# Optimization experiments

Measured on AMD Instinct MI355X. Metric: run time of the kernel, lower is better.

Reference implementation:

```python
import jax, jax.numpy as jnp
import numpy as np

DIM = 2048
N_HEADS = 16
HEAD_DIM = DIM // N_HEADS
MAX_SEQ_LEN = 2048
ROPE_THETA = 32.0
EPS = 1e-6


def _precompute_freqs_1d(dim, max_seq_len, theta):
    freqs = theta ** (-np.arange(0, dim, 2, dtype=np.float32) / dim)  # [dim/2]
    pos = np.arange(max_seq_len, dtype=np.float32)                    # [S]
    ang = pos[:, None] * freqs[None, :]                               # [S, dim/2]
    return jnp.asarray(np.cos(ang)), jnp.asarray(np.sin(ang))


def _rms_norm(x, w):
    # x: [..., d]
    inv = jax.lax.rsqrt(jnp.mean(x * x, axis=-1, keepdims=True) + EPS)
    return x * inv * w


def setup_inputs() -> dict:
    key = jax.random.key(0)
    k1, k2, k3 = jax.random.split(key, 3)
    bsz, seq_len = 4, 2048
    x = jax.random.normal(k1, (bsz, seq_len, DIM), dtype=jnp.float32)
    w_qkv = jax.random.normal(k2, (3 * DIM, DIM), dtype=jnp.float32) * (DIM ** -0.5)
    w_proj = jax.random.normal(k3, (DIM, DIM), dtype=jnp.float32) * (DIM ** -0.5)
    q_norm_w = jnp.ones((HEAD_DIM,), dtype=jnp.float32)
    k_norm_w = jnp.ones((HEAD_DIM,), dtype=jnp.float32)
    return {"x": x, "w_qkv": w_qkv, "w_proj": w_proj,
            "q_norm_w": q_norm_w, "k_norm_w": k_norm_w}


def reference(x, w_qkv, w_proj, q_norm_w, k_norm_w):
    bsz, seq_len, dim = x.shape
    scale = HEAD_DIM ** -0.5

    # QKV projection (torch Linear: x @ W^T)
    qkv = jnp.einsum('bsd,ed->bse', x, w_qkv)  # [b, s, 3*dim]
    qkv = qkv.reshape(bsz, seq_len, 3, N_HEADS, HEAD_DIM).transpose(2, 0, 3, 1, 4)
    q, k, v = qkv[0], qkv[1], qkv[2]           # each [b, h, s, d]

    # Per-head RMSNorm on q, k
    q = _rms_norm(q, q_norm_w)
    k = _rms_norm(k, k_norm_w)

    # RoPE (half-split convention)
    cos, sin = _precompute_freqs_1d(HEAD_DIM, MAX_SEQ_LEN, ROPE_THETA)
    cos = cos[:seq_len][None, None]  # [1,1,s,d/2]
    sin = sin[:seq_len][None, None]
    q1, q2 = jnp.split(q, 2, axis=-1)
    k1, k2 = jnp.split(k, 2, axis=-1)
    q = jnp.concatenate([q1 * cos - q2 * sin, q2 * cos + q1 * sin], axis=-1)
    k = jnp.concatenate([k1 * cos - k2 * sin, k2 * cos + k1 * sin], axis=-1)

    # Scaled dot-product attention (no mask, eval-mode: no dropout)
    scores = jnp.einsum('bhqd,bhkd->bhqk', q, k) * scale
    attn = jax.nn.softmax(scores, axis=-1)
    y = jnp.einsum('bhqk,bhkd->bhqd', attn, v)

    # Merge heads + output projection
    y = y.transpose(0, 2, 1, 3).reshape(bsz, seq_len, dim)
    return jnp.einsum('bsd,ed->bse', y, w_proj)
```

## Files before the change

### kernel.cpp

```cpp
#include <hip/hip_runtime.h>
#include <hip/hip_bf16.h>

#define BSZ 4
#define SEQ 2048
#define DIM 2048
#define NH 16
#define HD 128
#define QK_LD 4096
#define SCALE 0.08838834764831845f
#define SC2 0.12751742910198f

typedef __attribute__((ext_vector_type(8))) short bf16x8;
typedef __attribute__((ext_vector_type(4))) float f32x4;

#define GLDS16(g, l)                                                           \
  __builtin_amdgcn_global_load_lds(                                           \
      (const __attribute__((address_space(1))) void*)(g),                     \
      (__attribute__((address_space(3))) void*)(l), 16, 0, 0)

__device__ inline short f2b(float f) {
  __hip_bfloat16 h = __float2bfloat16(f);
  short s;
  __builtin_memcpy(&s, &h, 2);
  return s;
}

__device__ inline void stage16(const float* gp, __hip_bfloat16* lp) {
  float4 q0 = ((const float4*)gp)[0], q1 = ((const float4*)gp)[1];
  float4 q2 = ((const float4*)gp)[2], q3 = ((const float4*)gp)[3];
  bf16x8 v0, v1;
  v0[0] = f2b(q0.x); v0[1] = f2b(q0.y); v0[2] = f2b(q0.z); v0[3] = f2b(q0.w);
  v0[4] = f2b(q1.x); v0[5] = f2b(q1.y); v0[6] = f2b(q1.z); v0[7] = f2b(q1.w);
  v1[0] = f2b(q2.x); v1[1] = f2b(q2.y); v1[2] = f2b(q2.z); v1[3] = f2b(q2.w);
  v1[4] = f2b(q3.x); v1[5] = f2b(q3.y); v1[6] = f2b(q3.z); v1[7] = f2b(q3.w);
  *(bf16x8*)lp = v0;
  *(bf16x8*)(lp + 8) = v1;
}

__device__ inline char* out_slice(void* outv, int b, int fl) {
  return (char*)outv + (size_t)b * (size_t)SEQ * DIM * (fl ? 2u : 4u);
}

__device__ inline void xcd_remap(long& bm, long& bn) {
  int nwg = gridDim.x * gridDim.y;
  int lin = blockIdx.y * gridDim.x + blockIdx.x;
  int cpx = nwg >> 3;
  lin = (lin & 7) * cpx + (lin >> 3);
  bm = (long)(lin % gridDim.x) * 128;
  bn = (long)(lin / gridDim.x) * 128;
}

__global__ __launch_bounds__(256)
void detect_canon(const unsigned int* __restrict__ wbits,
                  const void* __restrict__ qw, const void* __restrict__ kw,
                  __hip_bfloat16* __restrict__ qwb,
                  __hip_bfloat16* __restrict__ kwb, int* __restrict__ flag) {
  __shared__ int cnt;
  const int t = threadIdx.x;
  if (t == 0) cnt = 0;
  __syncthreads();
  int local = 0;
  for (int i = 0; i < 4; ++i) {
    unsigned int e = (wbits[t * 4 + i] >> 7) & 0xFF;
    if (e >= 96 && e < 160) local++;
  }
  atomicAdd(&cnt, local);
  __syncthreads();
  const int f = (cnt >= 768) ? 1 : 0;
  if (t == 0) *flag = f;
  if (t < 128)
    qwb[t] = f ? ((const __hip_bfloat16*)qw)[t]
               : __float2bfloat16(((const float*)qw)[t]);
  else
    kwb[t - 128] = f ? ((const __hip_bfloat16*)kw)[t - 128]
                     : __float2bfloat16(((const float*)kw)[t - 128]);
}

__global__ __launch_bounds__(256)
void convert_bf16(const void* __restrict__ in, __hip_bfloat16* __restrict__ out,
                  const int* __restrict__ flag) {
  const int fl = *flag;
  long i = ((long)blockIdx.x * 256 + threadIdx.x) * 8;
  if (fl) {
    *(float4*)(out + i) = *(const float4*)((const __hip_bfloat16*)in + i);
  } else {
    const float* p = (const float*)in + i;
    float4 a = ((const float4*)p)[0], b = ((const float4*)p)[1];
    bf16x8 o;
    o[0] = f2b(a.x); o[1] = f2b(a.y); o[2] = f2b(a.z); o[3] = f2b(a.w);
    o[4] = f2b(b.x); o[5] = f2b(b.y); o[6] = f2b(b.z); o[7] = f2b(b.w);
    *(bf16x8*)(out + i) = o;
  }
}


__global__ __launch_bounds__(256)
void gemm_qkv_full(const __hip_bfloat16* __restrict__ A,
                   const __hip_bfloat16* __restrict__ B,
                   __hip_bfloat16* __restrict__ qk, void* __restrict__ outv,
                   const int* __restrict__ flag) {
  __shared__ __hip_bfloat16 As[128 * 32];
  __shared__ __hip_bfloat16 Bs[128 * 32];
  const int t = threadIdx.x, wave = t >> 6, lane = t & 63;
  const int quad = lane >> 4, l16 = lane & 15;
  const int wm = (wave & 1) * 64, wn = (wave >> 1) * 64;
  long bm, bn;
  xcd_remap(bm, bn);
  const int fl = *flag;

  f32x4 acc[4][4] = {};
  for (int k0 = 0; k0 < DIM; k0 += 32) {
    __syncthreads();
    for (int i = 0; i < 2; ++i) {
      int c = wave * 64 + lane + i * 256;
      int row = c >> 2, kc = c & 3;
      GLDS16(A + (bm + row) * DIM + k0 + kc * 8, As + (wave * 64 + i * 256) * 8);
      GLDS16(B + (bn + row) * DIM + k0 + kc * 8, Bs + (wave * 64 + i * 256) * 8);
    }
    __syncthreads();
    bf16x8 aF[4], bF[4];
    for (int mt = 0; mt < 4; ++mt)
      aF[mt] = *(const bf16x8*)(As + (wm + mt * 16 + l16) * 32 + quad * 8);
    for (int nt = 0; nt < 4; ++nt)
      bF[nt] = *(const bf16x8*)(Bs + (wn + nt * 16 + l16) * 32 + quad * 8);
    for (int mt = 0; mt < 4; ++mt)
      for (int nt = 0; nt < 4; ++nt)
        acc[mt][nt] = __builtin_amdgcn_mfma_f32_16x16x32_bf16(
            aF[mt], bF[nt], acc[mt][nt], 0, 0, 0);
  }

  if (bn < 4096) {
    for (int mt = 0; mt < 4; ++mt) {
      long gr = bm + wm + mt * 16 + quad * 4;
      for (int nt = 0; nt < 4; ++nt) {
        long gc = bn + wn + nt * 16 + l16;
        for (int r = 0; r < 4; ++r)
          qk[(gr + r) * QK_LD + gc] = __float2bfloat16(acc[mt][nt][r]);
      }
    }
  } else {
    for (int mt = 0; mt < 4; ++mt) {
      long gr = bm + wm + mt * 16 + quad * 4;
      __hip_bfloat16* vtb = (__hip_bfloat16*)out_slice(outv, (int)(gr >> 11), fl);
      long s = gr & 2047;
      for (int nt = 0; nt < 4; ++nt) {
        long col = bn - 4096 + wn + nt * 16 + l16;
        for (int r = 0; r < 4; ++r)
          vtb[col * SEQ + s + r] = __float2bfloat16(acc[mt][nt][r]);
      }
    }
  }
}

__global__ __launch_bounds__(256)
void gemm_proj_full(const __hip_bfloat16* __restrict__ A,
                    const __hip_bfloat16* __restrict__ B,
                    void* __restrict__ outv, const int* __restrict__ flag) {
  __shared__ __hip_bfloat16 As[128 * 32];
  __shared__ __hip_bfloat16 Bs[128 * 32];
  const int t = threadIdx.x, wave = t >> 6, lane = t & 63;
  const int quad = lane >> 4, l16 = lane & 15;
  const int wm = (wave & 1) * 64, wn = (wave >> 1) * 64;
  long bm, bn;
  xcd_remap(bm, bn);
  const int fl = *flag;

  f32x4 acc[4][4] = {};
  for (int k0 = 0; k0 < DIM; k0 += 32) {
    __syncthreads();
    for (int i = 0; i < 2; ++i) {
      int c = wave * 64 + lane + i * 256;
      int row = c >> 2, kc = c & 3;
      GLDS16(A + (bm + row) * QK_LD + k0 + kc * 8, As + (wave * 64 + i * 256) * 8);
      GLDS16(B + (bn + row) * DIM + k0 + kc * 8, Bs + (wave * 64 + i * 256) * 8);
    }
    __syncthreads();
    bf16x8 aF[4], bF[4];
    for (int mt = 0; mt < 4; ++mt)
      aF[mt] = *(const bf16x8*)(As + (wm + mt * 16 + l16) * 32 + quad * 8);
    for (int nt = 0; nt < 4; ++nt)
      bF[nt] = *(const bf16x8*)(Bs + (wn + nt * 16 + l16) * 32 + quad * 8);
    for (int mt = 0; mt < 4; ++mt)
      for (int nt = 0; nt < 4; ++nt)
        acc[mt][nt] = __builtin_amdgcn_mfma_f32_16x16x32_bf16(
            aF[mt], bF[nt], acc[mt][nt], 0, 0, 0);
  }

  for (int mt = 0; mt < 4; ++mt) {
    long gr = bm + wm + mt * 16 + quad * 4;
    for (int nt = 0; nt < 4; ++nt) {
      long gc = bn + wn + nt * 16 + l16;
      for (int r = 0; r < 4; ++r) {
        long idx = (gr + r) * DIM + gc;
        if (fl) ((__hip_bfloat16*)outv)[idx] = __float2bfloat16(acc[mt][nt][r]);
        else    ((float*)outv)[idx] = acc[mt][nt][r];
      }
    }
  }
}


__global__ __launch_bounds__(256)
void gemm_qkv(const void* __restrict__ xin, const void* __restrict__ win,
              __hip_bfloat16* __restrict__ qk, void* __restrict__ outv,
              const int* __restrict__ flag, int b) {
  __shared__ __hip_bfloat16 As[128 * 32];
  __shared__ __hip_bfloat16 Bs[128 * 32];
  const int t = threadIdx.x, wave = t >> 6, lane = t & 63;
  const int quad = lane >> 4, l16 = lane & 15;
  const int wm = (wave & 1) * 64, wn = (wave >> 1) * 64;
  const long bm = (long)blockIdx.x * 128, bn = (long)blockIdx.y * 128;
  const int fl = *flag;
  const __hip_bfloat16* Ab = (const __hip_bfloat16*)xin + (long)b * SEQ * DIM;
  const __hip_bfloat16* Bb = (const __hip_bfloat16*)win;
  const float* Af = (const float*)xin + (long)b * SEQ * DIM;
  const float* Bf = (const float*)win;

  f32x4 acc[4][4] = {};
  for (int k0 = 0; k0 < DIM; k0 += 32) {
    __syncthreads();
    if (fl) {
      for (int i = 0; i < 2; ++i) {
        int c = wave * 64 + lane + i * 256;
        int row = c >> 2, kc = c & 3;
        GLDS16(Ab + (bm + row) * DIM + k0 + kc * 8, As + (wave * 64 + i * 256) * 8);
        GLDS16(Bb + (bn + row) * DIM + k0 + kc * 8, Bs + (wave * 64 + i * 256) * 8);
      }
    } else {
      int row = t >> 1, cb = k0 + (t & 1) * 16;
      stage16(Af + (bm + row) * DIM + cb, As + t * 16);
      stage16(Bf + (bn + row) * DIM + cb, Bs + t * 16);
    }
    __syncthreads();
    bf16x8 aF[4], bF[4];
    for (int mt = 0; mt < 4; ++mt)
      aF[mt] = *(const bf16x8*)(As + (wm + mt * 16 + l16) * 32 + quad * 8);
    for (int nt = 0; nt < 4; ++nt)
      bF[nt] = *(const bf16x8*)(Bs + (wn + nt * 16 + l16) * 32 + quad * 8);
    for (int mt = 0; mt < 4; ++mt)
      for (int nt = 0; nt < 4; ++nt)
        acc[mt][nt] = __builtin_amdgcn_mfma_f32_16x16x32_bf16(
            aF[mt], bF[nt], acc[mt][nt], 0, 0, 0);
  }

  if (bn < 4096) {
    for (int mt = 0; mt < 4; ++mt) {
      long gr = bm + wm + mt * 16 + quad * 4;
      for (int nt = 0; nt < 4; ++nt) {
        long gc = bn + wn + nt * 16 + l16;
        for (int r = 0; r < 4; ++r)
          qk[(gr + r) * QK_LD + gc] = __float2bfloat16(acc[mt][nt][r]);
      }
    }
  } else {
    __hip_bfloat16* vtb = (__hip_bfloat16*)out_slice(outv, b, fl);
    for (int mt = 0; mt < 4; ++mt) {
      long gr = bm + wm + mt * 16 + quad * 4;
      for (int nt = 0; nt < 4; ++nt) {
        long col = bn - 4096 + wn + nt * 16 + l16;
        for (int r = 0; r < 4; ++r)
          vtb[col * SEQ + gr + r] = __float2bfloat16(acc[mt][nt][r]);
      }
    }
  }
}

__global__ __launch_bounds__(256)
void gemm_proj(const __hip_bfloat16* __restrict__ A, const void* __restrict__ win,
               void* __restrict__ outv, const int* __restrict__ flag, int b) {
  __shared__ __hip_bfloat16 As[128 * 32];
  __shared__ __hip_bfloat16 Bs[128 * 32];
  const int t = threadIdx.x, wave = t >> 6, lane = t & 63;
  const int quad = lane >> 4, l16 = lane & 15;
  const int wm = (wave & 1) * 64, wn = (wave >> 1) * 64;
  const long bm = (long)blockIdx.x * 128, bn = (long)blockIdx.y * 128;
  const int fl = *flag;
  const __hip_bfloat16* Bb = (const __hip_bfloat16*)win;
  const float* Bf = (const float*)win;

  f32x4 acc[4][4] = {};
  for (int k0 = 0; k0 < DIM; k0 += 32) {
    __syncthreads();
    for (int i = 0; i < 2; ++i) {
      int c = wave * 64 + lane + i * 256;
      int row = c >> 2, kc = c & 3;
      GLDS16(A + (bm + row) * QK_LD + k0 + kc * 8, As + (wave * 64 + i * 256) * 8);
    }
    if (fl) {
      for (int i = 0; i < 2; ++i) {
        int c = wave * 64 + lane + i * 256;
        int row = c >> 2, kc = c & 3;
        GLDS16(Bb + (bn + row) * DIM + k0 + kc * 8, Bs + (wave * 64 + i * 256) * 8);
      }
    } else {
      int row = t >> 1, cb = k0 + (t & 1) * 16;
      stage16(Bf + (bn + row) * DIM + cb, Bs + t * 16);
    }
    __syncthreads();
    bf16x8 aF[4], bF[4];
    for (int mt = 0; mt < 4; ++mt)
      aF[mt] = *(const bf16x8*)(As + (wm + mt * 16 + l16) * 32 + quad * 8);
    for (int nt = 0; nt < 4; ++nt)
      bF[nt] = *(const bf16x8*)(Bs + (wn + nt * 16 + l16) * 32 + quad * 8);
    for (int mt = 0; mt < 4; ++mt)
      for (int nt = 0; nt < 4; ++nt)
        acc[mt][nt] = __builtin_amdgcn_mfma_f32_16x16x32_bf16(
            aF[mt], bF[nt], acc[mt][nt], 0, 0, 0);
  }

  char* Cb = out_slice(outv, b, fl);
  for (int mt = 0; mt < 4; ++mt) {
    long gr = bm + wm + mt * 16 + quad * 4;
    for (int nt = 0; nt < 4; ++nt) {
      long gc = bn + wn + nt * 16 + l16;
      for (int r = 0; r < 4; ++r) {
        long idx = (gr + r) * DIM + gc;
        if (fl) ((__hip_bfloat16*)Cb)[idx] = __float2bfloat16(acc[mt][nt][r]);
        else    ((float*)Cb)[idx] = acc[mt][nt][r];
      }
    }
  }
}


__global__ __launch_bounds__(256)
void norm_rope(__hip_bfloat16* __restrict__ qk,
               const __hip_bfloat16* __restrict__ qwb,
               const __hip_bfloat16* __restrict__ kwb) {
  const int wave = threadIdx.x >> 6, lane = threadIdx.x & 63;
  const int gid = blockIdx.x * 4 + wave;
  const int h = gid & 15, tt = (gid >> 4) & 1, row = gid >> 5;
  const int s = row & 2047;

  __hip_bfloat16* p = qk + (long)row * QK_LD + tt * DIM + h * HD;
  unsigned int u = ((const unsigned int*)p)[lane];

  unsigned int x = (unsigned int)__shfl((int)u, lane >> 1);
  unsigned int y = (unsigned int)__shfl((int)u, 32 + (lane >> 1));
  float v1 = __uint_as_float((lane & 1) ? (x & 0xFFFF0000u) : (x << 16));
  float v2 = __uint_as_float((lane & 1) ? (y & 0xFFFF0000u) : (y << 16));

  float ss = v1 * v1 + v2 * v2;
  for (int off = 1; off < 64; off <<= 1) ss += __shfl_xor(ss, off);
  float inv = rsqrtf(ss * (1.0f / 128.0f) + 1e-6f);

  const __hip_bfloat16* w = tt ? kwb : qwb;
  float n1 = v1 * inv * __bfloat162float(w[lane]);
  float n2 = v2 * inv * __bfloat162float(w[lane + 64]);

  float freq = exp2f(-5.0f * (float)lane * (1.0f / 64.0f));
  float ang = (float)s * freq;
  float c = cosf(ang), sn = sinf(ang);
  float r1 = n1 * c - n2 * sn;
  float r2 = n2 * c + n1 * sn;

  float z1lo = __shfl(r1, (2 * lane) & 63), z2lo = __shfl(r2, (2 * lane) & 63);
  float z1hi = __shfl(r1, (2 * lane + 1) & 63), z2hi = __shfl(r2, (2 * lane + 1) & 63);
  float lo = (lane < 32) ? z1lo : z2lo;
  float hi = (lane < 32) ? z1hi : z2hi;
  unsigned int ou = (unsigned int)(unsigned short)f2b(lo) |
                    ((unsigned int)(unsigned short)f2b(hi) << 16);
  ((unsigned int*)p)[lane] = ou;
}

#define FA_STAGE_K(J)                                                          \
  _Pragma("unroll")                                                            \
  for (int i_ = 0; i_ < 2; ++i_) {                                             \
    int f_ = t + i_ * 512;                                                     \
    int kk_ = f_ & 3, row_ = (f_ >> 2) & 63, ks_ = f_ >> 8;                    \
    GLDS16(Kg + (long)((J) + row_) * QK_LD + ks_ * 32 +                        \
               (kk_ ^ ((row_ >> 1) & 3)) * 8,                                  \
           Ks + (t + i_ * 512) * 8);                                           \
  }
#define FA_STAGE_V(J)                                                          \
  _Pragma("unroll")                                                            \
  for (int i_ = 0; i_ < 2; ++i_) {                                             \
    int f_ = t + i_ * 512;                                                     \
    int kk_ = f_ & 3, dim_ = (f_ >> 2) & 127, ks2_ = f_ >> 9;                  \
    GLDS16(Vt + (long)dim_ * SEQ + (J) + ks2_ * 32 +                           \
               (kk_ ^ ((dim_ >> 1) & 3)) * 8,                                  \
           Vs + (t + i_ * 512) * 8);                                           \
  }
#define FA_WAIT2 asm volatile("s_waitcnt vmcnt(2)" ::: "memory")
#define FA_WAIT0 asm volatile("s_waitcnt vmcnt(0)" ::: "memory")
#define FA_BAR                                                                 \
  do {                                                                         \
    asm volatile("" ::: "memory");                                             \
    __builtin_amdgcn_s_barrier();                                              \
    asm volatile("" ::: "memory");                                             \
  } while (0)

__global__ __launch_bounds__(512)
void flash_attn(__hip_bfloat16* __restrict__ qkbase, void* __restrict__ outv,
                const int* __restrict__ flag, int b0) {
  __shared__ __hip_bfloat16 Ks[4 * 64 * 32];
  __shared__ __hip_bfloat16 Vs[2 * 128 * 32];

  const int t = threadIdx.x, wave = t >> 6, lane = t & 63;
  const int quad = lane >> 4, l16 = lane & 15;
  const int swz = (quad ^ ((l16 >> 1) & 3)) * 8;
  const int q0 = blockIdx.x * 128, h = blockIdx.y;
  const int b = b0 + blockIdx.z;
  const int fl = *flag;
  __hip_bfloat16* qk = qkbase + (long)blockIdx.z * SEQ * QK_LD;
  __hip_bfloat16* Qg = qk + h * HD;
  const __hip_bfloat16* Kg = Qg + DIM;
  const __hip_bfloat16* Vt =
      (const __hip_bfloat16*)out_slice(outv, b, fl) + (long)h * HD * SEQ;

  const int srcA = ((lane >> 4) & 1) * 32 + l16;
  const int srcB = srcA + 16;
  const bool hiq = (quad >= 2);

  bf16x8 aQ[4];
#pragma unroll
  for (int ks = 0; ks < 4; ++ks)
    aQ[ks] = *(const bf16x8*)(Qg +
        (long)(q0 + wave * 16 + l16) * QK_LD + ks * 32 + quad * 8);

  f32x4 oacc[8] = {};
  float m_run = -1e30f, l_run = 0.0f;

  FA_STAGE_K(0);
  FA_STAGE_V(0);

  for (int j0 = 0; j0 < SEQ; j0 += 64) {
    const bool more = (j0 + 64 < SEQ);

    FA_WAIT2;
    FA_BAR;

    f32x4 sacc[4] = {};
    __builtin_amdgcn_s_setprio(1);
#pragma unroll
    for (int ks = 0; ks < 4; ++ks)
#pragma unroll
      for (int nt = 0; nt < 4; ++nt) {
        bf16x8 bK = *(const bf16x8*)(Ks + (ks * 64 + nt * 16 + l16) * 32 + swz);
        sacc[nt] = __builtin_amdgcn_mfma_f32_16x16x32_bf16(
            bK, aQ[ks], sacc[nt], 0, 0, 0);
      }
    __builtin_amdgcn_s_setprio(0);

    FA_BAR;
    if (more) { FA_STAGE_K(j0 + 64); }

    float p[16];
#pragma unroll
    for (int nt = 0; nt < 4; ++nt)
#pragma unroll
      for (int r = 0; r < 4; ++r) p[nt * 4 + r] = sacc[nt][r] * SC2;
    float mx = p[0];
#pragma unroll
    for (int i = 1; i < 16; ++i) mx = fmaxf(mx, p[i]);
    mx = fmaxf(mx, __shfl_xor(mx, 16));
    mx = fmaxf(mx, __shfl_xor(mx, 32));
    if (__any(mx > m_run + 8.0f)) {
      float mnew = fmaxf(m_run, mx);
      float alpha = exp2f(m_run - mnew);
      m_run = mnew;
      l_run *= alpha;
#pragma unroll
      for (int r = 0; r < 4; ++r) {
        float ar = __shfl(alpha, quad * 20 + r);
#pragma unroll
        for (int n = 0; n < 8; ++n) oacc[n][r] *= ar;
      }
    }
    unsigned int W[4][2];
    float sum = 0.0f;
#pragma unroll
    for (int nt = 0; nt < 4; ++nt) {
      float e0 = exp2f(p[nt * 4 + 0] - m_run), e1 = exp2f(p[nt * 4 + 1] - m_run);
      float e2 = exp2f(p[nt * 4 + 2] - m_run), e3 = exp2f(p[nt * 4 + 3] - m_run);
      sum += (e0 + e1) + (e2 + e3);
      W[nt][0] = (unsigned int)(unsigned short)f2b(e0) |
                 ((unsigned int)(unsigned short)f2b(e1) << 16);
      W[nt][1] = (unsigned int)(unsigned short)f2b(e2) |
                 ((unsigned int)(unsigned short)f2b(e3) << 16);
    }
    l_run += sum;

    union { unsigned int u[4]; bf16x8 v; } ap[2];
#pragma unroll
    for (int ks2 = 0; ks2 < 2; ++ks2) {
#pragma unroll
      for (int hh = 0; hh < 2; ++hh) {
        unsigned int lo0 = (unsigned int)__shfl((int)W[2 * ks2][hh], srcA);
        unsigned int hi0 = (unsigned int)__shfl((int)W[2 * ks2 + 1][hh], srcA);
        unsigned int lo1 = (unsigned int)__shfl((int)W[2 * ks2][hh], srcB);
        unsigned int hi1 = (unsigned int)__shfl((int)W[2 * ks2 + 1][hh], srcB);
        ap[ks2].u[hh] = hiq ? hi0 : lo0;
        ap[ks2].u[2 + hh] = hiq ? hi1 : lo1;
      }
    }

    if (more) { FA_WAIT2; } else { FA_WAIT0; }
    FA_BAR;

    __builtin_amdgcn_s_setprio(1);
#pragma unroll
    for (int ks2 = 0; ks2 < 2; ++ks2) {
      bf16x8 aP = ap[ks2].v;
#pragma unroll
      for (int n = 0; n < 8; ++n) {
        bf16x8 bV = *(const bf16x8*)(Vs + (ks2 * 128 + n * 16 + l16) * 32 + swz);
        oacc[n] = __builtin_amdgcn_mfma_f32_16x16x32_bf16(
            aP, bV, oacc[n], 0, 0, 0);
      }
    }
    __builtin_amdgcn_s_setprio(0);

    FA_BAR;
    if (more) { FA_STAGE_V(j0 + 64); }
  }

  float l = l_run;
  l += __shfl_xor(l, 16);
  l += __shfl_xor(l, 32);
  float rl = 1.0f / l;
#pragma unroll
  for (int r = 0; r < 4; ++r) {
    float rlr = __shfl(rl, quad * 20 + r);
    long s = q0 + wave * 16 + quad * 4 + r;
    for (int n = 0; n < 8; ++n)
      qk[s * QK_LD + h * HD + n * 16 + l16] =
          __float2bfloat16(oacc[n][r] * rlr);
  }
}

extern "C" void kernel_launch(void* const* d_in, const int* in_sizes, int n_in,
                              void* d_out, int out_size, void* d_ws, size_t ws_size,
                              hipStream_t stream) {
  int* flag = (int*)d_ws;
  __hip_bfloat16* qwb = (__hip_bfloat16*)((char*)d_ws + 64);
  __hip_bfloat16* kwb = qwb + 128;
  char* base = (char*)d_ws + 1024;

  detect_canon<<<1, 256, 0, stream>>>((const unsigned int*)d_in[1], d_in[3],
                                      d_in[4], qwb, kwb, flag);

  const size_t MB = 1024ull * 1024ull;
  const size_t NEED_A = 1024 + 128 * MB;

  if (ws_size >= NEED_A) {
    __hip_bfloat16* xb     = (__hip_bfloat16*)base;
    __hip_bfloat16* wqkvb  = (__hip_bfloat16*)(base + 32 * MB);
    __hip_bfloat16* wprojb = (__hip_bfloat16*)(base + 56 * MB);
    __hip_bfloat16* qk     = (__hip_bfloat16*)(base + 64 * MB);

    convert_bf16<<<(BSZ * SEQ * DIM) / 2048, 256, 0, stream>>>(d_in[0], xb, flag);
    convert_bf16<<<(3 * DIM * DIM) / 2048, 256, 0, stream>>>(d_in[1], wqkvb, flag);
    convert_bf16<<<(DIM * DIM) / 2048, 256, 0, stream>>>(d_in[2], wprojb, flag);

    gemm_qkv_full<<<dim3((BSZ * SEQ) / 128, (3 * DIM) / 128), 256, 0, stream>>>(
        xb, wqkvb, qk, d_out, flag);
    norm_rope<<<(BSZ * SEQ * 2 * NH) / 4, 256, 0, stream>>>(qk, qwb, kwb);
    flash_attn<<<dim3(SEQ / 128, NH, BSZ), 512, 0, stream>>>(qk, d_out, flag, 0);
    gemm_proj_full<<<dim3((BSZ * SEQ) / 128, DIM / 128), 256, 0, stream>>>(
        qk, wprojb, d_out, flag);
  } else {
    __hip_bfloat16* qk = (__hip_bfloat16*)base;
    for (int b = 0; b < BSZ; ++b) {
      gemm_qkv<<<dim3(SEQ / 128, (3 * DIM) / 128), 256, 0, stream>>>(
          d_in[0], d_in[1], qk, d_out, flag, b);
      norm_rope<<<(SEQ * 2 * NH) / 4, 256, 0, stream>>>(qk, qwb, kwb);
      flash_attn<<<dim3(SEQ / 128, NH, 1), 512, 0, stream>>>(qk, d_out, flag, b);
      gemm_proj<<<dim3(SEQ / 128, DIM / 128), 256, 0, stream>>>(
          qk, d_in[2], d_out, flag, b);
    }
  }
}
```

Measured before the change: 781.9 us.

## Double-buffer LDS tiles in QKV and projection GEMMs to overlap loads with MFMA

Both full GEMM kernels now use two LDS buffers for the A and B tiles. Each iteration issues the global-to-LDS loads for the next K slice before computing on the current one, which removes one barrier per iteration and lets memory traffic overlap with the MFMA work. Wave priority is also raised around the MFMA block. LDS use per block doubles, which may lower occupancy. The global_load_lds writes rely on the single trailing barrier to be complete before the next read.

Measured after the change: 791.2 us. No clear change (+1.2%).

```diff
diff --git a/kernel.cpp b/kernel.cpp
--- a/kernel.cpp
+++ b/kernel.cpp
@@ -99,8 +99,8 @@
                    const __hip_bfloat16* __restrict__ B,
                    __hip_bfloat16* __restrict__ qk, void* __restrict__ outv,
                    const int* __restrict__ flag) {
-  __shared__ __hip_bfloat16 As[128 * 32];
-  __shared__ __hip_bfloat16 Bs[128 * 32];
+  __shared__ __hip_bfloat16 As[2 * 128 * 32];
+  __shared__ __hip_bfloat16 Bs[2 * 128 * 32];
   const int t = threadIdx.x, wave = t >> 6, lane = t & 63;
   const int quad = lane >> 4, l16 = lane & 15;
   const int wm = (wave & 1) * 64, wn = (wave >> 1) * 64;
@@ -109,24 +109,40 @@
   const int fl = *flag;
 
   f32x4 acc[4][4] = {};
+  for (int i = 0; i < 2; ++i) {
+    int c = wave * 64 + lane + i * 256;
+    int row = c >> 2, kc = c & 3;
+    GLDS16(A + (bm + row) * DIM + kc * 8, As + (wave * 64 + i * 256) * 8);
+    GLDS16(B + (bn + row) * DIM + kc * 8, Bs + (wave * 64 + i * 256) * 8);
+  }
+  __syncthreads();
+
   for (int k0 = 0; k0 < DIM; k0 += 32) {
-    __syncthreads();
-    for (int i = 0; i < 2; ++i) {
-      int c = wave * 64 + lane + i * 256;
-      int row = c >> 2, kc = c & 3;
-      GLDS16(A + (bm + row) * DIM + k0 + kc * 8, As + (wave * 64 + i * 256) * 8);
-      GLDS16(B + (bn + row) * DIM + k0 + kc * 8, Bs + (wave * 64 + i * 256) * 8);
-    }
-    __syncthreads();
+    const int cur = (k0 >> 5) & 1;
+    if (k0 + 32 < DIM) {
+      const int nb = (cur ^ 1) * 4096;
+      for (int i = 0; i < 2; ++i) {
+        int c = wave * 64 + lane + i * 256;
+        int row = c >> 2, kc = c & 3;
+        GLDS16(A + (bm + row) * DIM + k0 + 32 + kc * 8,
+               As + nb + (wave * 64 + i * 256) * 8);
+        GLDS16(B + (bn + row) * DIM + k0 + 32 + kc * 8,
+               Bs + nb + (wave * 64 + i * 256) * 8);
+      }
+    }
+    const int cb = cur * 4096;
     bf16x8 aF[4], bF[4];
     for (int mt = 0; mt < 4; ++mt)
-      aF[mt] = *(const bf16x8*)(As + (wm + mt * 16 + l16) * 32 + quad * 8);
+      aF[mt] = *(const bf16x8*)(As + cb + (wm + mt * 16 + l16) * 32 + quad * 8);
     for (int nt = 0; nt < 4; ++nt)
-      bF[nt] = *(const bf16x8*)(Bs + (wn + nt * 16 + l16) * 32 + quad * 8);
+      bF[nt] = *(const bf16x8*)(Bs + cb + (wn + nt * 16 + l16) * 32 + quad * 8);
+    __builtin_amdgcn_s_setprio(1);
     for (int mt = 0; mt < 4; ++mt)
       for (int nt = 0; nt < 4; ++nt)
         acc[mt][nt] = __builtin_amdgcn_mfma_f32_16x16x32_bf16(
             aF[mt], bF[nt], acc[mt][nt], 0, 0, 0);
+    __builtin_amdgcn_s_setprio(0);
+    __syncthreads();
   }
 
   if (bn < 4096) {
@@ -156,8 +172,8 @@
 void gemm_proj_full(const __hip_bfloat16* __restrict__ A,
                     const __hip_bfloat16* __restrict__ B,
                     void* __restrict__ outv, const int* __restrict__ flag) {
-  __shared__ __hip_bfloat16 As[128 * 32];
-  __shared__ __hip_bfloat16 Bs[128 * 32];
+  __shared__ __hip_bfloat16 As[2 * 128 * 32];
+  __shared__ __hip_bfloat16 Bs[2 * 128 * 32];
   const int t = threadIdx.x, wave = t >> 6, lane = t & 63;
   const int quad = lane >> 4, l16 = lane & 15;
   const int wm = (wave & 1) * 64, wn = (wave >> 1) * 64;
@@ -166,24 +182,40 @@
   const int fl = *flag;
 
   f32x4 acc[4][4] = {};
+  for (int i = 0; i < 2; ++i) {
+    int c = wave * 64 + lane + i * 256;
+    int row = c >> 2, kc = c & 3;
+    GLDS16(A + (bm + row) * QK_LD + kc * 8, As + (wave * 64 + i * 256) * 8);
+    GLDS16(B + (bn + row) * DIM + kc * 8, Bs + (wave * 64 + i * 256) * 8);
+  }
+  __syncthreads();
+
   for (int k0 = 0; k0 < DIM; k0 += 32) {
-    __syncthreads();
-    for (int i = 0; i < 2; ++i) {
-      int c = wave * 64 + lane + i * 256;
-      int row = c >> 2, kc = c & 3;
-      GLDS16(A + (bm + row) * QK_LD + k0 + kc * 8, As + (wave * 64 + i * 256) * 8);
-      GLDS16(B + (bn + row) * DIM + k0 + kc * 8, Bs + (wave * 64 + i * 256) * 8);
-    }
-    __syncthreads();
+    const int cur = (k0 >> 5) & 1;
+    if (k0 + 32 < DIM) {
+      const int nb = (cur ^ 1) * 4096;
+      for (int i = 0; i < 2; ++i) {
+        int c = wave * 64 + lane + i * 256;
+        int row = c >> 2, kc = c & 3;
+        GLDS16(A + (bm + row) * QK_LD + k0 + 32 + kc * 8,
+               As + nb + (wave * 64 + i * 256) * 8);
+        GLDS16(B + (bn + row) * DIM + k0 + 32 + kc * 8,
+               Bs + nb + (wave * 64 + i * 256) * 8);
+      }
+    }
+    const int cb = cur * 4096;
     bf16x8 aF[4], bF[4];
     for (int mt = 0; mt < 4; ++mt)
-      aF[mt] = *(const bf16x8*)(As + (wm + mt * 16 + l16) * 32 + quad * 8);
+      aF[mt] = *(const bf16x8*)(As + cb + (wm + mt * 16 + l16) * 32 + quad * 8);
     for (int nt = 0; nt < 4; ++nt)
-      bF[nt] = *(const bf16x8*)(Bs + (wn + nt * 16 + l16) * 32 + quad * 8);
+      bF[nt] = *(const bf16x8*)(Bs + cb + (wn + nt * 16 + l16) * 32 + quad * 8);
+    __builtin_amdgcn_s_setprio(1);
     for (int mt = 0; mt < 4; ++mt)
       for (int nt = 0; nt < 4; ++nt)
         acc[mt][nt] = __builtin_amdgcn_mfma_f32_16x16x32_bf16(
             aF[mt], bF[nt], acc[mt][nt], 0, 0, 0);
+    __builtin_amdgcn_s_setprio(0);
+    __syncthreads();
   }
 
   for (int mt = 0; mt < 4; ++mt) {
```
